# Optimization experiments

Measured on AMD Instinct MI355X. Metric: run time of the kernel, lower is better.

The kernel has to match this reference:

```python
import jax, jax.numpy as jnp
import numpy as np

K = 9          # kernel taps along the space-filling curve
SIGMA = 1.0    # gaussian bandwidth (conv2 uses SIGMA * stride, stride=1)
EPS = 1e-5     # BatchNorm eps


def _weighted_conv(x, w, coords, indices, reindices, sigma):
    """Gather points into curve order, run a k-tap 1D conv whose taps are
    modulated by a Gaussian of coordinate distance, scatter back.
    x: [B,C,N], w: [O,C,K], coords: [B,3,N], indices/reindices: [B,N]."""
    B, C, N = x.shape
    pad = K // 2
    idx = indices[:, None, :]
    xp = jnp.take_along_axis(x, jnp.broadcast_to(idx, (B, C, N)), axis=2)        # curve order
    cp = jnp.take_along_axis(coords, jnp.broadcast_to(idx, (B, 3, N)), axis=2)
    x_pad = jnp.pad(xp, ((0, 0), (0, 0), (pad, pad)))
    c_pad = jnp.pad(cp, ((0, 0), (0, 0), (pad, pad)))
    inv_s2 = 1.0 / (sigma * sigma)
    out = jnp.zeros((B, w.shape[0], N), x.dtype)
    for t in range(K):  # small fixed loop over kernel taps
        xw = x_pad[:, :, t:t + N]                     # [B,C,N]
        rel = c_pad[:, :, t:t + N] - cp               # [B,3,N]
        g = jnp.exp(-jnp.sum(rel * rel, axis=1) * inv_s2)  # [B,N] gaussian weight
        out = out + jnp.einsum('oc,bcn->bon', w[:, :, t], xw * g[:, None, :])
    ridx = reindices[:, None, :]
    return jnp.take_along_axis(out, jnp.broadcast_to(ridx, out.shape), axis=2)


def _batchnorm1d(x, gamma, beta):
    # training-mode BN over (batch, points) per channel, biased variance
    mean = jnp.mean(x, axis=(0, 2), keepdims=True)
    var = jnp.mean((x - mean) ** 2, axis=(0, 2), keepdims=True)
    return gamma[None, :, None] * (x - mean) * jax.lax.rsqrt(var + EPS) + beta[None, :, None]


def setup_inputs() -> dict:
    key = jax.random.key(0)
    ks = jax.random.split(key, 6)
    B, C, N = 4, 128, 65536
    x = jax.random.normal(ks[0], (B, C, N), jnp.float32)
    coords = jax.random.uniform(ks[1], (B, 3, N), jnp.float32)
    perm = jnp.stack([jax.random.permutation(jax.random.fold_in(ks[2], b), N) for b in range(B)])
    indices = perm.astype(jnp.int32)
    reindices = jnp.argsort(perm, axis=1).astype(jnp.int32)
    w1 = jax.random.normal(ks[3], (C, C, K), jnp.float32) * 0.05
    w2 = jax.random.normal(ks[4], (C, C, K), jnp.float32) * 0.05
    gamma1 = jnp.ones((C,), jnp.float32)
    beta1 = jnp.zeros((C,), jnp.float32)
    gamma2 = jnp.ones((C,), jnp.float32)
    beta2 = jnp.zeros((C,), jnp.float32)
    return {"x": x, "coords": coords, "indices": indices, "reindices": reindices,
            "w1": w1, "gamma1": gamma1, "beta1": beta1,
            "w2": w2, "gamma2": gamma2, "beta2": beta2}


def reference(x, coords, indices, reindices, w1, gamma1, beta1, w2, gamma2, beta2):
    identity = x
    out = _weighted_conv(x, w1, coords, indices, reindices, SIGMA)
    out = jax.nn.relu(_batchnorm1d(out, gamma1, beta1))
    out = _weighted_conv(out, w2, coords, indices, reindices, SIGMA * 1)  # stride=1
    out = _batchnorm1d(out, gamma2, beta2)
    return jax.nn.relu(out + identity)
```

## Files before the change

### kernel.cpp

```cpp
#include <hip/hip_runtime.h>

#define Bn 4
#define Cn 128
#define Nn 65536
#define KT 9
#define T_OUT 256
#define T_HALO 264
#define XROW 136
#define GROW 264
#define FT 66

typedef _Float16 f16x8 __attribute__((ext_vector_type(8)));
typedef _Float16 f16x4 __attribute__((ext_vector_type(4)));
typedef float f32x4 __attribute__((ext_vector_type(4)));
typedef float f32x2 __attribute__((ext_vector_type(2)));

__global__ __launch_bounds__(256) void repack_w(const float* __restrict__ w1,
                                                const float* __restrict__ w2,
                                                _Float16* __restrict__ Wr) {
  int i = blockIdx.x * 256 + threadIdx.x;
  int c = i & 127;
  int o = (i >> 7) & 127;
  int t = (i >> 14) % KT;
  int cv = i / (KT << 14);
  const float* w = cv ? w2 : w1;
  Wr[i] = (_Float16)w[(o * 128 + c) * KT + t];
}

__global__ __launch_bounds__(256) void gather_x(const float* __restrict__ x,
                                                const int* __restrict__ reidx,
                                                _Float16* __restrict__ xp) {
  __shared__ float ft[128 * FT];
  int tid = threadIdx.x;
  int b = blockIdx.x >> 10;
  int n0 = (blockIdx.x & 1023) * 64;
  const float* xb = x + (size_t)b * Cn * Nn;
  {
    int cc = tid >> 4;
    int j4 = (tid & 15) * 4;
#pragma unroll
    for (int pass = 0; pass < 8; ++pass) {
      int c = pass * 16 + cc;
      f32x4 v = *(const f32x4*)(&xb[(size_t)c * Nn + n0 + j4]);
      *(f32x2*)(&ft[c * FT + j4]) = f32x2{v.x, v.y};
      *(f32x2*)(&ft[c * FT + j4 + 2]) = f32x2{v.z, v.w};
    }
  }
  __syncthreads();
  int ch = tid & 15;
  int rr = tid >> 4;
#pragma unroll
  for (int pass = 0; pass < 4; ++pass) {
    int r = pass * 16 + rr;
    int m = reidx[(size_t)b * Nn + n0 + r];
    f16x8 v;
#pragma unroll
    for (int k = 0; k < 8; ++k) v[k] = (_Float16)ft[(ch * 8 + k) * FT + r];
    *(f16x8*)(xp + ((size_t)b * Nn + m) * Cn + ch * 8) = v;
  }
}

__global__ __launch_bounds__(256) void gather_g(const float* __restrict__ coords,
                                                const int* __restrict__ indices,
                                                float* __restrict__ G) {
  __shared__ float cx[264], cy[264], cz[264];
  int tid = threadIdx.x;
  int b = blockIdx.x >> 8;
  int n0 = (blockIdx.x & 255) * 256;
  const float* cb = coords + (size_t)b * 3 * Nn;
  for (int i = tid; i < 264; i += 256) {
    int q = n0 - 4 + i;
    q = q < 0 ? 0 : (q > Nn - 1 ? Nn - 1 : q);
    int idx = indices[(size_t)b * Nn + q];
    cx[i] = cb[idx];
    cy[i] = cb[Nn + idx];
    cz[i] = cb[2 * Nn + idx];
  }
  __syncthreads();
  int m = n0 + tid;
  float x0 = cx[tid + 4], y0 = cy[tid + 4], z0 = cz[tid + 4];
  float* Gb = G + (size_t)b * KT * Nn;
#pragma unroll
  for (int t = 0; t < KT; ++t) {
    float dx = cx[tid + t] - x0;
    float dy = cy[tid + t] - y0;
    float dz = cz[tid + t] - z0;
    Gb[(size_t)t * Nn + m] = __expf(-(dx * dx + dy * dy + dz * dz));
  }
}

__global__ void bncoeff(const float* __restrict__ sums,
                        const float* __restrict__ gamma,
                        const float* __restrict__ beta,
                        float* __restrict__ coeff) {
  int c = threadIdx.x;
  const float inv = 1.0f / (float)((size_t)Bn * Nn);
  float mean = sums[c] * inv;
  float var = sums[128 + c] * inv - mean * mean;
  float a = gamma[c] * rsqrtf(var + 1e-5f);
  coeff[c] = a;
  coeff[128 + c] = beta[c] - mean * a;
}

__device__ __forceinline__ f16x8 scale8(f16x8 v, _Float16 g) {
  f16x8 r;
#pragma unroll
  for (int i = 0; i < 8; ++i) r[i] = v[i] * g;
  return r;
}

template <int TRANS>
__global__ __launch_bounds__(256, 2) void conv_mfma(
    const _Float16* __restrict__ Xin, const _Float16* __restrict__ W,
    const float* __restrict__ G, _Float16* __restrict__ Yout,
    float* __restrict__ sums, const float* __restrict__ coeff) {
  __shared__ __align__(16) _Float16 Xs[T_HALO * XROW];
  __shared__ __align__(16) unsigned char aux[KT * GROW * 2];
  _Float16* Gs = (_Float16*)aux;
  float* red = (float*)aux;

  const int tid = threadIdx.x;
  const int b = blockIdx.x >> 8;
  const int p0 = (blockIdx.x & 255) * T_OUT;
  const int ch = tid & 15;

#pragma unroll
  for (int pass = 0; pass < 17; ++pass) {
    int r = pass * 16 + (tid >> 4);
    if (r < T_HALO) {
      int q = p0 - 4 + r;
      f16x8 v = {0, 0, 0, 0, 0, 0, 0, 0};
      if (q >= 0 && q < Nn) {
        v = *(const f16x8*)(Xin + ((size_t)b * Nn + q) * Cn + ch * 8);
        if (TRANS) {
#pragma unroll
          for (int i = 0; i < 8; ++i) {
            float f = fmaxf(coeff[ch * 8 + i] * (float)v[i] + coeff[128 + ch * 8 + i], 0.f);
            v[i] = (_Float16)f;
          }
        }
      }
      *(f16x8*)(&Xs[r * XROW + ch * 8]) = v;
    }
  }
  {
    const float* gb = G + (size_t)b * KT * Nn + p0;
    for (int i = tid; i < KT * 256; i += 256) {
      int t = i >> 8;
      int p = i & 255;
      Gs[t * GROW + p] = (_Float16)gb[(size_t)t * Nn + p];
    }
  }

  const int w = tid >> 6;
  const int lane = tid & 63;
  const int l15 = lane & 15;
  const int quad = lane >> 4;
  const int wm = w >> 1;
  const int wn = w & 1;

  f32x4 acc[4][8];
  const f32x4 z4 = {0.f, 0.f, 0.f, 0.f};
#pragma unroll
  for (int mt = 0; mt < 4; ++mt)
#pragma unroll
    for (int nt = 0; nt < 8; ++nt) acc[mt][nt] = z4;

  __syncthreads();

#pragma unroll 1
  for (int t = 0; t < KT; ++t) {
    _Float16 gt[8];
#pragma unroll
    for (int nt = 0; nt < 8; ++nt)
      gt[nt] = Gs[t * GROW + wn * 128 + nt * 16 + l15];

    const _Float16* Wt = W + ((size_t)t << 14) + (wm * 64) * Cn;
#pragma unroll
    for (int ko = 0; ko < 4; ++ko) {
      f16x8 a[4];
#pragma unroll
      for (int mt = 0; mt < 4; ++mt)
        a[mt] = *(const f16x8*)(Wt + (mt * 16 + l15) * Cn + ko * 32 + quad * 8);
#pragma unroll
      for (int nt = 0; nt < 8; ++nt) {
        f16x8 bv = *(const f16x8*)(&Xs[(wn * 128 + nt * 16 + l15 + t) * XROW + ko * 32 + quad * 8]);
        bv = scale8(bv, gt[nt]);
#pragma unroll
        for (int mt = 0; mt < 4; ++mt)
          acc[mt][nt] = __builtin_amdgcn_mfma_f32_16x16x32_f16(a[mt], bv, acc[mt][nt], 0, 0, 0);
      }
    }
  }

  f32x4 s4[4], q4[4];
#pragma unroll
  for (int mt = 0; mt < 4; ++mt) {
#pragma unroll
    for (int rg = 0; rg < 4; ++rg) {
      float s = 0.f, q = 0.f;
#pragma unroll
      for (int nt = 0; nt < 8; ++nt) {
        float v = acc[mt][nt][rg];
        s += v;
        q += v * v;
      }
#pragma unroll
      for (int m = 1; m < 16; m <<= 1) {
        s += __shfl_xor(s, m);
        q += __shfl_xor(q, m);
      }
      s4[mt][rg] = s;
      q4[mt][rg] = q;
    }
  }
  __syncthreads();
  if (l15 == 0) {
#pragma unroll
    for (int mt = 0; mt < 4; ++mt) {
      int cbase = wm * 64 + mt * 16 + quad * 4;
      *(f32x4*)(&red[wn * 128 + cbase]) = s4[mt];
      *(f32x4*)(&red[256 + wn * 128 + cbase]) = q4[mt];
    }
  }

  _Float16* Os = Xs;
#pragma unroll
  for (int mt = 0; mt < 4; ++mt)
#pragma unroll
    for (int nt = 0; nt < 8; ++nt) {
      f16x4 o4;
#pragma unroll
      for (int rg = 0; rg < 4; ++rg) o4[rg] = (_Float16)acc[mt][nt][rg];
      *(f16x4*)(&Os[(wn * 128 + nt * 16 + l15) * XROW + wm * 64 + mt * 16 + quad * 4]) = o4;
    }
  __syncthreads();

  if (tid < 128) {
    atomicAdd(&sums[tid], red[tid] + red[128 + tid]);
    atomicAdd(&sums[128 + tid], red[256 + tid] + red[384 + tid]);
  }
#pragma unroll
  for (int pass = 0; pass < 16; ++pass) {
    int r = pass * 16 + (tid >> 4);
    f16x8 v = *(const f16x8*)(&Os[r * XROW + ch * 8]);
    *(f16x8*)(Yout + ((size_t)b * Nn + p0 + r) * Cn + ch * 8) = v;
  }
}

__global__ __launch_bounds__(512, 4) void conv_mfma8(
    const _Float16* __restrict__ Xin, const _Float16* __restrict__ W,
    const float* __restrict__ G, _Float16* __restrict__ Yout,
    float* __restrict__ sums) {
  __shared__ __align__(16) _Float16 Xs[T_HALO * XROW];
  __shared__ __align__(16) unsigned char aux[KT * GROW * 2];
  _Float16* Gs = (_Float16*)aux;
  float* red = (float*)aux;

  const int tid = threadIdx.x;
  const int b = blockIdx.x >> 8;
  const int p0 = (blockIdx.x & 255) * T_OUT;
  const int ch = tid & 15;

#pragma unroll
  for (int pass = 0; pass < 9; ++pass) {
    int r = pass * 32 + (tid >> 4);
    if (r < T_HALO) {
      int q = p0 - 4 + r;
      f16x8 v = {0, 0, 0, 0, 0, 0, 0, 0};
      if (q >= 0 && q < Nn)
        v = *(const f16x8*)(Xin + ((size_t)b * Nn + q) * Cn + ch * 8);
      *(f16x8*)(&Xs[r * XROW + ch * 8]) = v;
    }
  }
  {
    const float* gb = G + (size_t)b * KT * Nn + p0;
    for (int i = tid; i < KT * 256; i += 512) {
      int t = i >> 8;
      int p = i & 255;
      Gs[t * GROW + p] = (_Float16)gb[(size_t)t * Nn + p];
    }
  }

  const int w = tid >> 6;
  const int lane = tid & 63;
  const int l15 = lane & 15;
  const int quad = lane >> 4;
  const int wm = w >> 2;
  const int wn = w & 3;

  f32x4 acc[4][4];
  const f32x4 z4 = {0.f, 0.f, 0.f, 0.f};
#pragma unroll
  for (int mt = 0; mt < 4; ++mt)
#pragma unroll
    for (int nt = 0; nt < 4; ++nt) acc[mt][nt] = z4;

  __syncthreads();

#pragma unroll 1
  for (int t = 0; t < KT; ++t) {
    _Float16 gt[4];
#pragma unroll
    for (int nt = 0; nt < 4; ++nt)
      gt[nt] = Gs[t * GROW + wn * 64 + nt * 16 + l15];

    const _Float16* Wt = W + ((size_t)t << 14) + (wm * 64) * Cn;
#pragma unroll
    for (int ko = 0; ko < 4; ++ko) {
      f16x8 a4[4];
#pragma unroll
      for (int mt = 0; mt < 4; ++mt)
        a4[mt] = *(const f16x8*)(Wt + (mt * 16 + l15) * Cn + ko * 32 + quad * 8);
#pragma unroll
      for (int nt = 0; nt < 4; ++nt) {
        f16x8 bv = *(const f16x8*)(&Xs[(wn * 64 + nt * 16 + l15 + t) * XROW + ko * 32 + quad * 8]);
        bv = scale8(bv, gt[nt]);
#pragma unroll
        for (int mt = 0; mt < 4; ++mt)
          acc[mt][nt] = __builtin_amdgcn_mfma_f32_16x16x32_f16(a4[mt], bv, acc[mt][nt], 0, 0, 0);
      }
    }
  }

  f32x4 s4[4], q4[4];
#pragma unroll
  for (int mt = 0; mt < 4; ++mt) {
#pragma unroll
    for (int rg = 0; rg < 4; ++rg) {
      float s = 0.f, q = 0.f;
#pragma unroll
      for (int nt = 0; nt < 4; ++nt) {
        float v = acc[mt][nt][rg];
        s += v;
        q += v * v;
      }
#pragma unroll
      for (int m = 1; m < 16; m <<= 1) {
        s += __shfl_xor(s, m);
        q += __shfl_xor(q, m);
      }
      s4[mt][rg] = s;
      q4[mt][rg] = q;
    }
  }
  __syncthreads();
  if (l15 == 0) {
#pragma unroll
    for (int mt = 0; mt < 4; ++mt) {
      int cbase = wm * 64 + mt * 16 + quad * 4;
      *(f32x4*)(&red[wn * 128 + cbase]) = s4[mt];
      *(f32x4*)(&red[512 + wn * 128 + cbase]) = q4[mt];
    }
  }

  _Float16* Os = Xs;
#pragma unroll
  for (int mt = 0; mt < 4; ++mt)
#pragma unroll
    for (int nt = 0; nt < 4; ++nt) {
      f16x4 o4;
#pragma unroll
      for (int rg = 0; rg < 4; ++rg) o4[rg] = (_Float16)acc[mt][nt][rg];
      *(f16x4*)(&Os[(wn * 64 + nt * 16 + l15) * XROW + wm * 64 + mt * 16 + quad * 4]) = o4;
    }
  __syncthreads();

  if (tid < 128) {
    atomicAdd(&sums[tid],
              red[tid] + red[128 + tid] + red[256 + tid] + red[384 + tid]);
    atomicAdd(&sums[128 + tid],
              red[512 + tid] + red[640 + tid] + red[768 + tid] + red[896 + tid]);
  }
#pragma unroll
  for (int pass = 0; pass < 8; ++pass) {
    int r = pass * 32 + (tid >> 4);
    f16x8 v = *(const f16x8*)(&Os[r * XROW + ch * 8]);
    *(f16x8*)(Yout + ((size_t)b * Nn + p0 + r) * Cn + ch * 8) = v;
  }
}

__global__ __launch_bounds__(256) void final_k(const _Float16* __restrict__ y2,
                                               const float* __restrict__ x,
                                               const int* __restrict__ reidx,
                                               const float* __restrict__ coeff,
                                               float* __restrict__ out) {
  __shared__ float ft[128 * FT];
  int tid = threadIdx.x;
  int b = blockIdx.x >> 10;
  int n0 = (blockIdx.x & 1023) * 64;
  {
    int ch = tid & 15;
#pragma unroll
    for (int pass = 0; pass < 4; ++pass) {
      int r = pass * 16 + (tid >> 4);
      int m = reidx[(size_t)b * Nn + n0 + r];
      f16x8 v = *(const f16x8*)(y2 + ((size_t)b * Nn + m) * Cn + ch * 8);
#pragma unroll
      for (int k = 0; k < 8; ++k) ft[(ch * 8 + k) * FT + r] = (float)v[k];
    }
  }
  __syncthreads();
  int cc = tid >> 4;
  int j4 = (tid & 15) * 4;
#pragma unroll
  for (int pass = 0; pass < 8; ++pass) {
    int c = pass * 16 + cc;
    float a = coeff[c];
    float bb = coeff[128 + c];
    f32x2 v0 = *(const f32x2*)(&ft[c * FT + j4]);
    f32x2 v1 = *(const f32x2*)(&ft[c * FT + j4 + 2]);
    size_t gi = ((size_t)b * Cn + c) * Nn + n0 + j4;
    f32x4 xv = *(const f32x4*)(&x[gi]);
    f32x4 r;
    r.x = fmaxf(a * v0.x + bb + xv.x, 0.f);
    r.y = fmaxf(a * v0.y + bb + xv.y, 0.f);
    r.z = fmaxf(a * v1.x + bb + xv.z, 0.f);
    r.w = fmaxf(a * v1.y + bb + xv.w, 0.f);
    *(f32x4*)(&out[gi]) = r;
  }
}

extern "C" void kernel_launch(void* const* d_in, const int* in_sizes, int n_in,
                              void* d_out, int out_size, void* d_ws, size_t ws_size,
                              hipStream_t stream) {
  (void)in_sizes; (void)n_in; (void)out_size; (void)ws_size;
  const float* x = (const float*)d_in[0];
  const float* coords = (const float*)d_in[1];
  const int* indices = (const int*)d_in[2];
  const int* reindices = (const int*)d_in[3];
  const float* w1 = (const float*)d_in[4];
  const float* gamma1 = (const float*)d_in[5];
  const float* beta1 = (const float*)d_in[6];
  const float* w2 = (const float*)d_in[7];
  const float* gamma2 = (const float*)d_in[8];
  const float* beta2 = (const float*)d_in[9];
  float* out = (float*)d_out;

  char* ws = (char*)d_ws;
  const size_t BUF0 = (size_t)Bn * Nn * Cn * sizeof(_Float16);
  _Float16* buf0 = (_Float16*)ws;
  float* sums1 = (float*)(ws + BUF0);
  float* sums2 = sums1 + 256;
  float* coeff1 = sums1 + 512;
  float* coeff2 = sums1 + 768;
  _Float16* Wr = (_Float16*)(ws + BUF0 + 4096);

  char* dob = (char*)d_out;
  _Float16* y1 = (_Float16*)dob;
  float* G = (float*)(dob + BUF0);

  hipMemsetAsync(sums1, 0, 512 * sizeof(float), stream);

  repack_w<<<1152, 256, 0, stream>>>(w1, w2, Wr);
  gather_x<<<Bn * 1024, 256, 0, stream>>>(x, reindices, buf0);
  gather_g<<<Bn * 256, 256, 0, stream>>>(coords, indices, G);

  conv_mfma8<<<Bn * 256, 512, 0, stream>>>(buf0, Wr, G, y1, sums1);
  bncoeff<<<1, 128, 0, stream>>>(sums1, gamma1, beta1, coeff1);
  conv_mfma<1><<<Bn * 256, 256, 0, stream>>>(y1, Wr + (size_t)KT * Cn * Cn, G,
                                             buf0, sums2, coeff1);
  bncoeff<<<1, 128, 0, stream>>>(sums2, gamma2, beta2, coeff2);
  final_k<<<Bn * 1024, 256, 0, stream>>>(buf0, x, reindices, coeff2, out);
}
```

Measured before the change: 616.7 us.

## Stage conv1 weights through double-buffered LDS and retile warps to 2x8 MFMA tiles

```diff
diff --git a/kernel.cpp b/kernel.cpp
--- a/kernel.cpp
+++ b/kernel.cpp
@@ -248,11 +248,12 @@
   }
 }
 
-__global__ __launch_bounds__(512, 4) void conv_mfma8(
+__global__ __launch_bounds__(512) void conv_wlds(
     const _Float16* __restrict__ Xin, const _Float16* __restrict__ W,
     const float* __restrict__ G, _Float16* __restrict__ Yout,
     float* __restrict__ sums) {
   __shared__ __align__(16) _Float16 Xs[T_HALO * XROW];
+  __shared__ __align__(16) _Float16 Wlds[2][128 * XROW];
   __shared__ __align__(16) unsigned char aux[KT * GROW * 2];
   _Float16* Gs = (_Float16*)aux;
   float* red = (float*)aux;
@@ -261,6 +262,14 @@
   const int b = blockIdx.x >> 8;
   const int p0 = (blockIdx.x & 255) * T_OUT;
   const int ch = tid & 15;
+
+  f16x8 w0r[4], w1r[4];
+#pragma unroll
+  for (int i = 0; i < 4; ++i) {
+    int q = i * 512 + tid;
+    w0r[i] = *(const f16x8*)(W + (q >> 4) * 128 + (q & 15) * 8);
+    w1r[i] = *(const f16x8*)(W + 16384 + (q >> 4) * 128 + (q & 15) * 8);
+  }
 
 #pragma unroll
   for (int pass = 0; pass < 9; ++pass) {
@@ -281,56 +290,81 @@
       Gs[t * GROW + p] = (_Float16)gb[(size_t)t * Nn + p];
     }
   }
+#pragma unroll
+  for (int i = 0; i < 4; ++i) {
+    int q = i * 512 + tid;
+    *(f16x8*)(&Wlds[0][(q >> 4) * XROW + (q & 15) * 8]) = w0r[i];
+    *(f16x8*)(&Wlds[1][(q >> 4) * XROW + (q & 15) * 8]) = w1r[i];
+  }
 
   const int w = tid >> 6;
   const int lane = tid & 63;
   const int l15 = lane & 15;
   const int quad = lane >> 4;
-  const int wm = w >> 2;
-  const int wn = w & 3;
-
-  f32x4 acc[4][4];
+  const int wm = w >> 1;
+  const int wn = w & 1;
+
+  f32x4 acc[2][8];
   const f32x4 z4 = {0.f, 0.f, 0.f, 0.f};
 #pragma unroll
-  for (int mt = 0; mt < 4; ++mt)
-#pragma unroll
-    for (int nt = 0; nt < 4; ++nt) acc[mt][nt] = z4;
-
-  __syncthreads();
-
+  for (int mt = 0; mt < 2; ++mt)
+#pragma unroll
+    for (int nt = 0; nt < 8; ++nt) acc[mt][nt] = z4;
+
+  __syncthreads();
+
+  f16x8 wpre[4];
 #pragma unroll 1
   for (int t = 0; t < KT; ++t) {
-    _Float16 gt[4];
-#pragma unroll
-    for (int nt = 0; nt < 4; ++nt)
-      gt[nt] = Gs[t * GROW + wn * 64 + nt * 16 + l15];
-
-    const _Float16* Wt = W + ((size_t)t << 14) + (wm * 64) * Cn;
+    if (t <= KT - 3) {
+      const _Float16* Wt2 = W + ((size_t)(t + 2) << 14);
+#pragma unroll
+      for (int i = 0; i < 4; ++i) {
+        int q = i * 512 + tid;
+        wpre[i] = *(const f16x8*)(Wt2 + (q >> 4) * 128 + (q & 15) * 8);
+      }
+    }
+
+    _Float16 gt[8];
+#pragma unroll
+    for (int nt = 0; nt < 8; ++nt)
+      gt[nt] = Gs[t * GROW + wn * 128 + nt * 16 + l15];
+
+    const _Float16* Wb = &Wlds[t & 1][0];
 #pragma unroll
     for (int ko = 0; ko < 4; ++ko) {
-      f16x8 a4[4];
-#pragma unroll
-      for (int mt = 0; mt < 4; ++mt)
-        a4[mt] = *(const f16x8*)(Wt + (mt * 16 + l15) * Cn + ko * 32 + quad * 8);
-#pragma unroll
-      for (int nt = 0; nt < 4; ++nt) {
-        f16x8 bv = *(const f16x8*)(&Xs[(wn * 64 + nt * 16 + l15 + t) * XROW + ko * 32 + quad * 8]);
+      f16x8 a2[2];
+#pragma unroll
+      for (int mt = 0; mt < 2; ++mt)
+        a2[mt] = *(const f16x8*)(Wb + (wm * 32 + mt * 16 + l15) * XROW + ko * 32 + quad * 8);
+#pragma unroll
+      for (int nt = 0; nt < 8; ++nt) {
+        f16x8 bv = *(const f16x8*)(&Xs[(wn * 128 + nt * 16 + l15 + t) * XROW + ko * 32 + quad * 8]);
         bv = scale8(bv, gt[nt]);
 #pragma unroll
-        for (int mt = 0; mt < 4; ++mt)
-          acc[mt][nt] = __builtin_amdgcn_mfma_f32_16x16x32_f16(a4[mt], bv, acc[mt][nt], 0, 0, 0);
-      }
-    }
-  }
-
-  f32x4 s4[4], q4[4];
-#pragma unroll
-  for (int mt = 0; mt < 4; ++mt) {
+        for (int mt = 0; mt < 2; ++mt)
+          acc[mt][nt] = __builtin_amdgcn_mfma_f32_16x16x32_f16(a2[mt], bv, acc[mt][nt], 0, 0, 0);
+      }
+    }
+
+    __syncthreads();
+    if (t <= KT - 3) {
+#pragma unroll
+      for (int i = 0; i < 4; ++i) {
+        int q = i * 512 + tid;
+        *(f16x8*)(&Wlds[t & 1][(q >> 4) * XROW + (q & 15) * 8]) = wpre[i];
+      }
+    }
+  }
+
+  f32x4 s4[2], q4[2];
+#pragma unroll
+  for (int mt = 0; mt < 2; ++mt) {
 #pragma unroll
     for (int rg = 0; rg < 4; ++rg) {
       float s = 0.f, q = 0.f;
 #pragma unroll
-      for (int nt = 0; nt < 4; ++nt) {
+      for (int nt = 0; nt < 8; ++nt) {
         float v = acc[mt][nt][rg];
         s += v;
         q += v * v;
@@ -344,33 +378,30 @@
       q4[mt][rg] = q;
     }
   }
-  __syncthreads();
   if (l15 == 0) {
 #pragma unroll
-    for (int mt = 0; mt < 4; ++mt) {
-      int cbase = wm * 64 + mt * 16 + quad * 4;
+    for (int mt = 0; mt < 2; ++mt) {
+      int cbase = wm * 32 + mt * 16 + quad * 4;
       *(f32x4*)(&red[wn * 128 + cbase]) = s4[mt];
-      *(f32x4*)(&red[512 + wn * 128 + cbase]) = q4[mt];
+      *(f32x4*)(&red[256 + wn * 128 + cbase]) = q4[mt];
     }
   }
 
   _Float16* Os = Xs;
 #pragma unroll
-  for (int mt = 0; mt < 4; ++mt)
-#pragma unroll
-    for (int nt = 0; nt < 4; ++nt) {
+  for (int mt = 0; mt < 2; ++mt)
+#pragma unroll
+    for (int nt = 0; nt < 8; ++nt) {
       f16x4 o4;
 #pragma unroll
       for (int rg = 0; rg < 4; ++rg) o4[rg] = (_Float16)acc[mt][nt][rg];
-      *(f16x4*)(&Os[(wn * 64 + nt * 16 + l15) * XROW + wm * 64 + mt * 16 + quad * 4]) = o4;
+      *(f16x4*)(&Os[(wn * 128 + nt * 16 + l15) * XROW + wm * 32 + mt * 16 + quad * 4]) = o4;
     }
   __syncthreads();
 
   if (tid < 128) {
-    atomicAdd(&sums[tid],
-              red[tid] + red[128 + tid] + red[256 + tid] + red[384 + tid]);
-    atomicAdd(&sums[128 + tid],
-              red[512 + tid] + red[640 + tid] + red[768 + tid] + red[896 + tid]);
+    atomicAdd(&sums[tid], red[tid] + red[128 + tid]);
+    atomicAdd(&sums[128 + tid], red[256 + tid] + red[384 + tid]);
   }
 #pragma unroll
   for (int pass = 0; pass < 8; ++pass) {
@@ -456,7 +487,7 @@
   gather_x<<<Bn * 1024, 256, 0, stream>>>(x, reindices, buf0);
   gather_g<<<Bn * 256, 256, 0, stream>>>(coords, indices, G);
 
-  conv_mfma8<<<Bn * 256, 512, 0, stream>>>(buf0, Wr, G, y1, sums1);
+  conv_wlds<<<Bn * 256, 512, 0, stream>>>(buf0, Wr, G, y1, sums1);
   bncoeff<<<1, 128, 0, stream>>>(sums1, gamma1, beta1, coeff1);
   conv_mfma<1><<<Bn * 256, 256, 0, stream>>>(y1, Wr + (size_t)KT * Cn * Cn, G,
                                              buf0, sums2, coeff1);
```

After: 555.9 us. 1.11x faster.
